# Kernel optimization log

Hardware: AMD Instinct MI355X
Metric: run time of the kernel (lower is better)

The kernel has to match this reference:

```python
import jax, jax.numpy as jnp
import numpy as np

B, TXT_T, MEL_T, N_MEL = 32, 256, 1600, 40
PAD_MAG = 1.0e12


def setup_inputs() -> dict:
    key = jax.random.key(0)
    k1, k2, k3, k4 = jax.random.split(key, 4)
    mu_logvar = jax.random.normal(k1, (B, TXT_T, 2 * N_MEL), jnp.float32)
    z = jax.random.normal(k2, (B, N_MEL, MEL_T), jnp.float32)
    text_lengths = jax.random.randint(k3, (B,), TXT_T // 2, TXT_T + 1).astype(jnp.int32)
    mel_lengths = jax.random.randint(k4, (B,), MEL_T // 2, MEL_T + 1).astype(jnp.int32)
    return {"mu_logvar": mu_logvar, "z": z,
            "text_lengths": text_lengths, "mel_lengths": mel_lengths}


def _mdn_log_prob(mu_logvar, z):
    # mu_logvar: [B, L, 2C], z: [B, C, T] -> log_prob_matrix [B, L, T]
    C = z.shape[1]
    mu, logvar = jnp.split(mu_logvar, 2, axis=-1)          # [B, L, C] each
    invvar = jnp.exp(-logvar)                               # [B, L, C]
    # mean_c((z - mu)^2 * invvar) expanded via matmuls (no [B,L,T,C] tensor)
    t1 = jnp.einsum('bct,blc->blt', z * z, invvar)
    t2 = jnp.einsum('bct,blc->blt', z, mu * invvar)
    t3 = jnp.sum(mu * mu * invvar, axis=-1)[:, :, None]
    mse = t1 - 2.0 * t2 + t3                                # [B, L, T]
    return -0.5 * (mse / C + jnp.mean(logvar, axis=-1)[:, :, None])


def _forward_dp(lp):
    # forward algorithm: log_alpha over (txt position, mel time) via scan over T
    Bb, L, T = lp.shape
    alpha0 = jnp.full((Bb, L + 1), -PAD_MAG, lp.dtype).at[:, 1].set(lp[:, 0, 0])

    def step(alpha, lp_t):
        stay = alpha[:, 1:] + 1e-7
        go = alpha[:, :-1] + 1e-7
        new = jnp.logaddexp(stay, go) + lp_t                # [B, L]
        alpha_new = jnp.concatenate(
            [jnp.full((Bb, 1), -PAD_MAG, lp.dtype), new], axis=1)
        return alpha_new, new

    _, ys = jax.lax.scan(step, alpha0, jnp.moveaxis(lp[:, :, 1:], 2, 0))
    log_alpha = jnp.concatenate([alpha0[:, 1:][None], ys], axis=0)  # [T, B, L]
    return log_alpha


def _viterbi(lp, text_lengths, mel_lengths):
    Bb, L, T = lp.shape
    beta0 = jnp.full((Bb, L), -PAD_MAG, lp.dtype).at[:, 0].set(lp[:, 0, 0])

    def fstep(beta, lp_t):
        shifted = jnp.concatenate(
            [jnp.full((Bb, 1), -PAD_MAG, lp.dtype), beta[:, :-1]], axis=1)
        new = jnp.maximum(beta, shifted) + lp_t
        return new, new

    _, ys = jax.lax.scan(fstep, beta0, jnp.moveaxis(lp[:, :, 1:], 2, 0))
    log_beta = jnp.transpose(jnp.concatenate([beta0[None], ys], axis=0), (1, 2, 0))  # [B, L, T]

    b_idx = jnp.arange(Bb)
    r0 = (text_lengths - 1).astype(jnp.float32)
    c0 = (mel_lengths - 1).astype(jnp.float32)

    def bstep(carry, _):
        rows, cols = carry
        ri = rows.astype(jnp.int32)
        ci = cols.astype(jnp.int32)
        # torch negative indexing wraps -> emulate with mod
        val_go = log_beta[b_idx, (ri - 1) % L, (ci - 1) % T]
        val_stay = log_beta[b_idx, ri % L, (ci - 1) % T]
        is_go = (val_go > val_stay).astype(rows.dtype)
        new_rows = jax.nn.relu(rows - is_go + 1.0) - 1.0
        new_cols = jax.nn.relu(cols) - 1.0
        return (new_rows, new_cols), new_rows

    _, path_ys = jax.lax.scan(bstep, (r0, c0), None, length=T - 1)
    full = jnp.concatenate([r0[None], path_ys], axis=0)     # [T, B], backward order
    path = full[::-1].T                                     # [B, T], chronological
    align = jax.nn.one_hot(path.astype(jnp.int32), L, dtype=lp.dtype)  # [B, T, L]

    def shift(a, ml):
        # F.pad(..., (-pad, pad)) on time axis: shift valid region to the front
        rolled = jnp.roll(a, -(T - ml), axis=0)
        mask = (jnp.arange(T) < ml)[:, None].astype(a.dtype)
        return rolled * mask

    return jax.vmap(shift)(align, mel_lengths)              # [B, T, L]


def reference(mu_logvar, z, text_lengths, mel_lengths):
    lp = _mdn_log_prob(mu_logvar, z)                        # [B, L, T]
    log_alpha = _forward_dp(lp)                             # [T, B, L]
    b_idx = jnp.arange(lp.shape[0])
    alpha_last = log_alpha[mel_lengths - 1, b_idx, text_lengths - 1]
    mdn_loss = -(alpha_last / mel_lengths.astype(alpha_last.dtype))  # [B]
    alignment = _viterbi(lp, text_lengths, mel_lengths)     # [B, T, L]
    return mdn_loss, alignment, lp
```

## Files before the change

kernel.cpp:

```cpp
#include <hip/hip_runtime.h>
#include <cstdint>
#include <math.h>

#define BB   32
#define LLEN 256
#define TLEN 1600
#define NC   40
#define NEGPADF (-1.0e12f)
#define NEGPADD (-1.0e12)
#define NBB   16
#define NBA   32
#define SUBB  8
#define NPROD 4
#define NBUF  3

#define LOG2E_F 1.4426950408889634f
#define LN2_F   0.6931471805599453f
#define C7F     1.4426950408889634e-7f

#define OFF_ALIGN 32
#define OFF_LP    (32 + (size_t)BB * TLEN * LLEN)

#define WSB_A    0
#define WSB_KC   (WSB_A + (size_t)BB * LLEN * 80 * 8)
#define WSB_LPT  (WSB_KC + (size_t)BB * LLEN * 8)

__device__ __forceinline__ int imin(int a, int b) { return a < b ? a : b; }

#define WAIT_LGKM0 0xC07F

__device__ __forceinline__ void bar_prod() {
  asm volatile("" ::: "memory");
  __builtin_amdgcn_s_waitcnt(WAIT_LGKM0);
  __builtin_amdgcn_s_barrier();
  asm volatile("" ::: "memory");
}
__device__ __forceinline__ void bar_cons() {
  asm volatile("" ::: "memory");
  __builtin_amdgcn_s_barrier();
  asm volatile("" ::: "memory");
}

__device__ __forceinline__ int rot1_i32(int x) {
  return __builtin_amdgcn_mov_dpp(x, 0x13C , 0xF, 0xF, true);
}
__device__ __forceinline__ float rot1_f32(float x) {
  return __int_as_float(rot1_i32(__float_as_int(x)));
}
__device__ __forceinline__ double rot1_f64(double x) {
  long long v = __double_as_longlong(x);
  int lo = rot1_i32((int)(v & 0xffffffffLL));
  int hi = rot1_i32((int)(v >> 32));
  return __longlong_as_double(((long long)hi << 32) | (unsigned long long)(unsigned int)lo);
}

__global__ __launch_bounds__(256) void prep_kernel(
    const float* __restrict__ mu_logvar, double* __restrict__ A, double* __restrict__ Kc) {
  int row = blockIdx.x * 4 + (threadIdx.x >> 6);
  int lane = threadIdx.x & 63;
  const float* src = mu_logvar + (size_t)row * (2 * NC);
  double mu = 0.0, lv = 0.0, iv = 0.0, part = 0.0;
  if (lane < NC) {
    mu = (double)src[lane];
    lv = (double)src[NC + lane];
    iv = exp(-lv);
    part = mu * mu * iv + lv;
  }
  for (int m = 1; m < 64; m <<= 1) part += __shfl_xor(part, m, 64);
  const double s = -0.5 / (double)NC;
  if (lane < NC) {
    A[(size_t)row * 80 + lane]      = s * iv;
    A[(size_t)row * 80 + NC + lane] = (1.0 / (double)NC) * mu * iv;
  }
  if (lane == 0) Kc[row] = s * part;
}

__global__ __launch_bounds__(128) void lp_kernel(
    const float* __restrict__ z, const double* __restrict__ A,
    const double* __restrict__ Kc, float* __restrict__ out,
    float* __restrict__ lpTh) {
  int b  = blockIdx.z;
  int l0 = blockIdx.y * 32;
  int t0 = blockIdx.x * 128;
  int tid = threadIdx.x;
  int t = t0 + tid;
  int tv = imin(t, TLEN - 1);
  bool act = (t < TLEN);

  float* lp_out = out + OFF_LP;
  float* loS    = out + OFF_ALIGN;

  float zr[NC];
  const float* zb = z + (size_t)b * NC * TLEN;
  #pragma unroll
  for (int c = 0; c < NC; ++c) zr[c] = zb[(size_t)c * TLEN + tv];

  __shared__ __align__(16) double tile[128][17];
  const double* Ab = A + ((size_t)b * LLEN + l0) * 80;
  const double* Kb = Kc + (size_t)b * LLEN + l0;

  for (int g = 0; g < 2; ++g) {
    for (int j16 = 0; j16 < 16; ++j16) {
      int j = g * 16 + j16;
      const double* Ar = Ab + (size_t)j * 80;
      double a0 = Kb[j], a1 = 0.0, a2 = 0.0, a3 = 0.0;
      #pragma unroll
      for (int c = 0; c < NC; c += 2) {
        double z0 = (double)zr[c], z1 = (double)zr[c + 1];
        a0 = fma(Ar[c],          z0 * z0, a0);
        a1 = fma(Ar[NC + c],     z0,      a1);
        a2 = fma(Ar[c + 1],      z1 * z1, a2);
        a3 = fma(Ar[NC + c + 1], z1,      a3);
      }
      double accd = (a0 + a2) + (a1 + a3);
      if (act) lp_out[((size_t)b * LLEN + l0 + j) * TLEN + t] = (float)accd;
      tile[tid][j16] = accd;
    }
    __syncthreads();
    #pragma unroll
    for (int p = 0; p < 4; ++p) {
      int idx = p * 128 + tid;
      int r = idx >> 2, c4 = idx & 3;
      int tr = t0 + r;
      if (tr < TLEN) {
        float h[4], lo[4];
        #pragma unroll
        for (int i = 0; i < 4; ++i) {
          double d = tile[r][c4 * 4 + i];
          float hh = (float)d;
          h[i] = hh;
          lo[i] = (float)(d - (double)hh);
        }
        size_t base = ((size_t)b * TLEN + tr) * LLEN + l0 + g * 16 + c4 * 4;
        *(float4*)(lpTh + base) = make_float4(h[0], h[1], h[2], h[3]);
        *(float4*)(loS + base)  = make_float4(lo[0], lo[1], lo[2], lo[3]);
      }
    }
    __syncthreads();
  }
}

__global__ __launch_bounds__(320, 1) void dp_kernel(
    const float* __restrict__ lpTh, const float* outR,
    const int* __restrict__ tlen, const int* __restrict__ mlen,
    float* __restrict__ out) {
  int bid = blockIdx.x;
  bool is_beta = (bid >= BB);
  int b = is_beta ? bid - BB : bid;
  int tid = threadIdx.x;
  int lane = tid & 63;
  int wv = tid >> 6;
  int tl = tlen[b];
  int ml = mlen[b];
  const float* lpb = lpTh + (size_t)b * TLEN * LLEN;
  const float* lob = outR + OFF_ALIGN + (size_t)b * TLEN * LLEN;
  float* al = out + OFF_ALIGN + (size_t)b * TLEN * LLEN;
  int nintB = (ml - 2 + NBB) / NBB;
  int nintA = (ml - 2 + NBA) / NBA;

  __shared__ __align__(16) double bufd[NBUF][NBB][4][64];
  __shared__ uint32_t Dbits[LLEN][TLEN / 32];
  __shared__ int pathL[TLEN];
  float* bufaF = (float*)&bufd[0][0][0][0];

  if (wv >= 1) {
    int q = wv - 1;
    const float* ph = lpb + 4 * lane;
    const float* pl = lob + 4 * lane;
    float4 vh[SUBB], vl[SUBB];
    float4 z4 = make_float4(0.f, 0.f, 0.f, 0.f);
    if (!is_beta) {
      int nsb = 4 * nintA;
      auto issueA = [&](int sb) {
        #pragma unroll
        for (int j = 0; j < SUBB; ++j) {
          int c = imin(1 + SUBB * sb + j, TLEN - 1);
          vh[j] = *(const float4*)(ph + (size_t)c * LLEN);
        }
      };
      auto storeA = [&](int sb) {
        int s  = (sb >> 2) % NBUF;
        int jb = (sb & 3) * SUBB;
        #pragma unroll
        for (int j = 0; j < SUBB; ++j) {
          int off = ((s * NBA + jb + j) * 4) * 64 + lane;
          bufaF[off]       = fmaf(vh[j].x, LOG2E_F, C7F);
          bufaF[off + 64]  = fmaf(vh[j].y, LOG2E_F, C7F);
          bufaF[off + 128] = fmaf(vh[j].z, LOG2E_F, C7F);
          bufaF[off + 192] = fmaf(vh[j].w, LOG2E_F, C7F);
        }
      };
      if (q < nsb)     { issueA(q);     storeA(q); }
      if (q + 4 < nsb) { issueA(q + 4); storeA(q + 4); }
      if (q + 8 < nsb) issueA(q + 8);
      bar_prod();
      for (int w = 0; w < nintA; ++w) {
        bar_prod();
        int S = 4 * (w + 2) + q;
        if (S < nsb) {
          storeA(S);
          if (S + 4 < nsb) issueA(S + 4);
        }
      }
    } else {
      int nsb = 2 * nintB;
      auto issueB = [&](int sb) {
        #pragma unroll
        for (int j = 0; j < SUBB; ++j) {
          int c = imin(1 + SUBB * sb + j, TLEN - 1);
          vh[j] = *(const float4*)(ph + (size_t)c * LLEN);
          vl[j] = *(const float4*)(pl + (size_t)c * LLEN);
        }
      };
      auto storeB = [&](int sb) {
        int s  = (sb >> 1) % NBUF;
        int jb = (sb & 1) * SUBB;
        #pragma unroll
        for (int j = 0; j < SUBB; ++j) {
          bufd[s][jb + j][0][lane] = (double)vh[j].x + (double)vl[j].x;
          bufd[s][jb + j][1][lane] = (double)vh[j].y + (double)vl[j].y;
          bufd[s][jb + j][2][lane] = (double)vh[j].z + (double)vl[j].z;
          bufd[s][jb + j][3][lane] = (double)vh[j].w + (double)vl[j].w;
        }
      };
      if (q < nsb) {
        issueB(q); storeB(q);
        if (q + NPROD < nsb) issueB(q + NPROD);
      }
      bar_prod();
      for (int w = 0; w < nintB; ++w) {
        bar_prod();
        int sb0 = 2 * w + 4;
        int mine = ((sb0 & 3) == q) ? sb0 : ((((sb0 + 1) & 3) == q) ? (sb0 + 1) : -1);
        if (mine >= 0 && mine < nsb) {
          storeB(mine);
          if (mine + NPROD < nsb) issueB(mine + NPROD);
        }
        if (w >= 1) {
          int zc = NBB * (w - 1) + 4 * q;
          float* az = al + (size_t)zc * LLEN + 4 * lane;
          #pragma unroll
          for (int k = 0; k < 4; ++k) *(float4*)(az + (size_t)k * LLEN) = z4;
        }
      }
      for (int c = NBB * (nintB - 1) + q; c < TLEN; c += NPROD)
        *(float4*)(al + (size_t)c * LLEN + 4 * lane) = z4;
    }
  } else if (!is_beta) {
    float lp00 = lpb[0] * LOG2E_F;
    float o0 = (lane == 0) ? lp00 : NEGPADF;
    float o1 = NEGPADF, o2 = NEGPADF, o3 = NEGPADF;
    float f0 = o0, f1 = o1, f2 = o2, f3 = o3;
    float qv = rot1_f32(o3);
    bar_cons();
    float P[4][4];
    #pragma unroll
    for (int i = 0; i < 4; ++i) {
      const float* src = bufaF + i * 256;
      P[i][0] = src[lane]; P[i][1] = src[64 + lane];
      P[i][2] = src[128 + lane]; P[i][3] = src[192 + lane];
    }
    int t = 1;
    for (int w = 0; w < nintA; ++w) {
      bar_cons();
      int s = w % NBUF, sn = (w + 1) % NBUF;
      const float* baseS = bufaF + s * (NBA * 256);
      const float* baseN = bufaF + sn * (NBA * 256);
      #pragma unroll
      for (int j = 0; j < NBA; ++j, ++t) {
        int rj = j & 3;
        float l0 = P[rj][0], l1 = P[rj][1], l2 = P[rj][2], l3 = P[rj][3];
        const float* src = (j < NBA - 4) ? (baseS + (j + 4) * 256)
                                         : (baseN + (j + 4 - NBA) * 256);
        P[rj][0] = src[lane];       P[rj][1] = src[64 + lane];
        P[rj][2] = src[128 + lane]; P[rj][3] = src[192 + lane];
        float p = (lane == 0) ? NEGPADF : qv;
        float m0 = fmaxf(o0, p),  d0 = o0 - p;
        float m1 = fmaxf(o1, o0), d1 = o1 - o0;
        float m2 = fmaxf(o2, o1), d2 = o2 - o1;
        float m3 = fmaxf(o3, o2), d3 = o3 - o2;
        float n0 = m0 + __builtin_amdgcn_logf(1.0f + __builtin_amdgcn_exp2f(-fabsf(d0))) + l0;
        float n1 = m1 + __builtin_amdgcn_logf(1.0f + __builtin_amdgcn_exp2f(-fabsf(d1))) + l1;
        float n2 = m2 + __builtin_amdgcn_logf(1.0f + __builtin_amdgcn_exp2f(-fabsf(d2))) + l2;
        float n3 = m3 + __builtin_amdgcn_logf(1.0f + __builtin_amdgcn_exp2f(-fabsf(d3))) + l3;
        o0 = n0; o1 = n1; o2 = n2; o3 = n3;
        qv = rot1_f32(o3);
        if (t == ml - 1) { f0 = o0; f1 = o1; f2 = o2; f3 = o3; }
      }
    }
    int fr = tl - 1;
    if (lane == (fr >> 2)) {
      int sx = fr & 3;
      float val = (sx == 0) ? f0 : (sx == 1) ? f1 : (sx == 2) ? f2 : f3;
      out[b] = -val * LN2_F / (float)ml;
    }
  } else {
    double lp00 = (double)lpb[0] + (double)lob[0];
    double o0 = (lane == 0) ? lp00 : NEGPADD;
    double o1 = NEGPADD, o2 = NEGPADD, o3 = NEGPADD;
    uint32_t a0 = 0, a1 = (lane == 0) ? 1u : 0u, a2 = 0, a3 = 0;
    double qv = rot1_f64(o3);
    bar_cons();
    double P[4][4];
    #pragma unroll
    for (int i = 0; i < 4; ++i) {
      P[i][0] = bufd[0][i][0][lane]; P[i][1] = bufd[0][i][1][lane];
      P[i][2] = bufd[0][i][2][lane]; P[i][3] = bufd[0][i][3][lane];
    }
    int t = 1;
    for (int w = 0; w < nintB; ++w) {
      bar_cons();
      int s = w % NBUF, sn = (w + 1) % NBUF;
      const double (*bs)[4][64] = bufd[s];
      const double (*bn)[4][64] = bufd[sn];
      #pragma unroll
      for (int j = 0; j < NBB; ++j, ++t) {
        int rj = j & 3;
        double l0 = P[rj][0], l1 = P[rj][1], l2 = P[rj][2], l3 = P[rj][3];
        {
          const double (*src)[64] = (j < NBB - 4) ? bs[j + 4] : bn[j + 4 - NBB];
          P[rj][0] = src[0][lane]; P[rj][1] = src[1][lane];
          P[rj][2] = src[2][lane]; P[rj][3] = src[3][lane];
        }
        double p = (lane == 0) ? NEGPADD : qv;
        double n0 = fmax(o0, p)  + l0;
        double n1 = fmax(o1, o0) + l1;
        double n2 = fmax(o2, o1) + l2;
        double n3 = fmax(o3, o2) + l3;
        qv = rot1_f64(n3);
        uint32_t bit = 1u << (t & 31);
        if (qv > n0) a0 |= bit;
        if (n0 > n1) a1 |= bit;
        if (n1 > n2) a2 |= bit;
        if (n2 > n3) a3 |= bit;
        o0 = n0; o1 = n1; o2 = n2; o3 = n3;
        if ((t & 31) == 31) {
          int wd = t >> 5;
          Dbits[4 * lane + 0][wd] = a0; a0 = 0;
          Dbits[4 * lane + 1][wd] = a1; a1 = 0;
          Dbits[4 * lane + 2][wd] = a2; a2 = 0;
          Dbits[4 * lane + 3][wd] = a3; a3 = 0;
        }
      }
    }
    int tend = nintB * NBB;
    int wd = tend >> 5;
    if ((tend & 31) != 31 && wd < TLEN / 32) {
      Dbits[4 * lane + 0][wd] = a0;
      Dbits[4 * lane + 1][wd] = a1;
      Dbits[4 * lane + 2][wd] = a2;
      Dbits[4 * lane + 3][wd] = a3;
    }
    __builtin_amdgcn_s_waitcnt(WAIT_LGKM0);

    if (lane == 0) {
      int r = tl - 1;
      pathL[ml - 1] = r;
      int curR = 1 << 30, curW = -1;
      uint32_t W = 0;
      for (int qq = ml - 2; qq >= 0; --qq) {
        int w2 = qq >> 5;
        if (r >= 0 && (r != curR || w2 != curW)) { W = Dbits[r][w2]; curR = r; curW = w2; }
        int g = (r >= 0) ? (int)((W >> (qq & 31)) & 1u) : 0;
        r -= g;
        pathL[qq] = r;
      }
    }
  }

  if (is_beta) {
    __syncthreads();
    for (int t = tid; t < ml; t += 320) {
      int p = pathL[t];
      if (p >= 0) al[(size_t)t * LLEN + p] = 1.0f;
    }
  }
}

extern "C" void kernel_launch(void* const* d_in, const int* in_sizes, int n_in,
                              void* d_out, int out_size, void* d_ws, size_t ws_size,
                              hipStream_t stream) {
  const float* mu_logvar = (const float*)d_in[0];
  const float* z         = (const float*)d_in[1];
  const int*   tlv       = (const int*)d_in[2];
  const int*   mlv       = (const int*)d_in[3];
  float* out = (float*)d_out;
  char*  wsb = (char*)d_ws;

  double* Ad   = (double*)(wsb + WSB_A);
  double* Kcd  = (double*)(wsb + WSB_KC);
  float*  lpTh = (float*)(wsb + WSB_LPT);

  prep_kernel<<<dim3(BB * LLEN / 4), 256, 0, stream>>>(mu_logvar, Ad, Kcd);
  lp_kernel<<<dim3(13, 8, BB), 128, 0, stream>>>(z, Ad, Kcd, out, lpTh);
  dp_kernel<<<dim3(2 * BB), 320, 0, stream>>>(lpTh, out, tlv, mlv, out);
}
```

Measured before the change: 496.5 us.

## Replace producer/consumer barriers with LDS flag polling in DP kernel

Swaps the workgroup-wide s_barrier handshakes between the four producer waves and the consumer wave for per-producer progress counters and a consumer progress counter in LDS. Each side spin-waits with s_sleep on those counters. The forward (alpha) path also drops its 32-step window and uses the same 16-step window and sub-block indexing as the Viterbi path. The goal is to let producers run ahead and stop the serial DP wave stalling at every window barrier. The cost is polling overhead and a dependence on volatile LDS ordering being correct.

```diff
diff --git a/kernel.cpp b/kernel.cpp
--- a/kernel.cpp
+++ b/kernel.cpp
@@ -9,7 +9,6 @@
 #define NEGPADF (-1.0e12f)
 #define NEGPADD (-1.0e12)
 #define NBB   16
-#define NBA   32
 #define SUBB  8
 #define NPROD 4
 #define NBUF  3
@@ -28,18 +27,6 @@
 __device__ __forceinline__ int imin(int a, int b) { return a < b ? a : b; }
 
 #define WAIT_LGKM0 0xC07F
-
-__device__ __forceinline__ void bar_prod() {
-  asm volatile("" ::: "memory");
-  __builtin_amdgcn_s_waitcnt(WAIT_LGKM0);
-  __builtin_amdgcn_s_barrier();
-  asm volatile("" ::: "memory");
-}
-__device__ __forceinline__ void bar_cons() {
-  asm volatile("" ::: "memory");
-  __builtin_amdgcn_s_barrier();
-  asm volatile("" ::: "memory");
-}
 
 __device__ __forceinline__ int rot1_i32(int x) {
   return __builtin_amdgcn_mov_dpp(x, 0x13C , 0xF, 0xF, true);
@@ -155,13 +142,19 @@
   const float* lpb = lpTh + (size_t)b * TLEN * LLEN;
   const float* lob = outR + OFF_ALIGN + (size_t)b * TLEN * LLEN;
   float* al = out + OFF_ALIGN + (size_t)b * TLEN * LLEN;
-  int nintB = (ml - 2 + NBB) / NBB;
-  int nintA = (ml - 2 + NBA) / NBA;
+  int nint = (ml - 2 + NBB) / NBB;
+  int nsb  = 2 * nint;
 
   __shared__ __align__(16) double bufd[NBUF][NBB][4][64];
   __shared__ uint32_t Dbits[LLEN][TLEN / 32];
   __shared__ int pathL[TLEN];
+  __shared__ int prodSb_s[NPROD];
+  __shared__ int consW_s;
   float* bufaF = (float*)&bufd[0][0][0][0];
+
+  if (tid < NPROD) prodSb_s[tid] = 0;
+  if (tid == NPROD) consW_s = 0;
+  __syncthreads();
 
   if (wv >= 1) {
     int q = wv - 1;
@@ -169,8 +162,8 @@
     const float* pl = lob + 4 * lane;
     float4 vh[SUBB], vl[SUBB];
     float4 z4 = make_float4(0.f, 0.f, 0.f, 0.f);
+    int myCnt = 0;
     if (!is_beta) {
-      int nsb = 4 * nintA;
       auto issueA = [&](int sb) {
         #pragma unroll
         for (int j = 0; j < SUBB; ++j) {
@@ -179,31 +172,33 @@
         }
       };
       auto storeA = [&](int sb) {
-        int s  = (sb >> 2) % NBUF;
-        int jb = (sb & 3) * SUBB;
+        int s  = (sb >> 1) % NBUF;
+        int jb = (sb & 1) * SUBB;
         #pragma unroll
         for (int j = 0; j < SUBB; ++j) {
-          int off = ((s * NBA + jb + j) * 4) * 64 + lane;
+          int off = ((s * NBB + jb + j) * 4) * 64 + lane;
           bufaF[off]       = fmaf(vh[j].x, LOG2E_F, C7F);
           bufaF[off + 64]  = fmaf(vh[j].y, LOG2E_F, C7F);
           bufaF[off + 128] = fmaf(vh[j].z, LOG2E_F, C7F);
           bufaF[off + 192] = fmaf(vh[j].w, LOG2E_F, C7F);
         }
       };
-      if (q < nsb)     { issueA(q);     storeA(q); }
-      if (q + 4 < nsb) { issueA(q + 4); storeA(q + 4); }
-      if (q + 8 < nsb) issueA(q + 8);
-      bar_prod();
-      for (int w = 0; w < nintA; ++w) {
-        bar_prod();
-        int S = 4 * (w + 2) + q;
-        if (S < nsb) {
-          storeA(S);
-          if (S + 4 < nsb) issueA(S + 4);
-        }
+      if (q < nsb) issueA(q);
+      for (int sb = q; sb < nsb; sb += 4) {
+        int u = sb >> 1;
+        if (u >= 3) {
+          while (*(volatile int*)&consW_s < u - 2) __builtin_amdgcn_s_sleep(2);
+        }
+        asm volatile("" ::: "memory");
+        storeA(sb);
+        asm volatile("" ::: "memory");
+        __builtin_amdgcn_s_waitcnt(WAIT_LGKM0);
+        ++myCnt;
+        if (lane == 0) *(volatile int*)&prodSb_s[q] = myCnt;
+        asm volatile("" ::: "memory");
+        if (sb + 4 < nsb) issueA(sb + 4);
       }
     } else {
-      int nsb = 2 * nintB;
       auto issueB = [&](int sb) {
         #pragma unroll
         for (int j = 0; j < SUBB; ++j) {
@@ -223,147 +218,168 @@
           bufd[s][jb + j][3][lane] = (double)vh[j].w + (double)vl[j].w;
         }
       };
-      if (q < nsb) {
-        issueB(q); storeB(q);
-        if (q + NPROD < nsb) issueB(q + NPROD);
-      }
-      bar_prod();
-      for (int w = 0; w < nintB; ++w) {
-        bar_prod();
-        int sb0 = 2 * w + 4;
-        int mine = ((sb0 & 3) == q) ? sb0 : ((((sb0 + 1) & 3) == q) ? (sb0 + 1) : -1);
-        if (mine >= 0 && mine < nsb) {
-          storeB(mine);
-          if (mine + NPROD < nsb) issueB(mine + NPROD);
-        }
-        if (w >= 1) {
-          int zc = NBB * (w - 1) + 4 * q;
+      if (q < nsb) issueB(q);
+      for (int sb = q; sb < nsb; sb += 4) {
+        int u = sb >> 1;
+        if (u >= 3) {
+          while (*(volatile int*)&consW_s < u - 2) __builtin_amdgcn_s_sleep(2);
+        }
+        asm volatile("" ::: "memory");
+        storeB(sb);
+        asm volatile("" ::: "memory");
+        __builtin_amdgcn_s_waitcnt(WAIT_LGKM0);
+        ++myCnt;
+        if (lane == 0) *(volatile int*)&prodSb_s[q] = myCnt;
+        asm volatile("" ::: "memory");
+        if (sb + 4 < nsb) issueB(sb + 4);
+        if (u >= 2) {
+          int zc = NBB * (u - 2) + 8 * (q & 1);
           float* az = al + (size_t)zc * LLEN + 4 * lane;
           #pragma unroll
-          for (int k = 0; k < 4; ++k) *(float4*)(az + (size_t)k * LLEN) = z4;
-        }
-      }
-      for (int c = NBB * (nintB - 1) + q; c < TLEN; c += NPROD)
+          for (int k = 0; k < 8; ++k) *(float4*)(az + (size_t)k * LLEN) = z4;
+        }
+      }
+      for (int c = NBB * (nint - 2) + q; c < TLEN; c += NPROD)
         *(float4*)(al + (size_t)c * LLEN + 4 * lane) = z4;
     }
-  } else if (!is_beta) {
-    float lp00 = lpb[0] * LOG2E_F;
-    float o0 = (lane == 0) ? lp00 : NEGPADF;
-    float o1 = NEGPADF, o2 = NEGPADF, o3 = NEGPADF;
-    float f0 = o0, f1 = o1, f2 = o2, f3 = o3;
-    float qv = rot1_f32(o3);
-    bar_cons();
-    float P[4][4];
-    #pragma unroll
-    for (int i = 0; i < 4; ++i) {
-      const float* src = bufaF + i * 256;
-      P[i][0] = src[lane]; P[i][1] = src[64 + lane];
-      P[i][2] = src[128 + lane]; P[i][3] = src[192 + lane];
-    }
-    int t = 1;
-    for (int w = 0; w < nintA; ++w) {
-      bar_cons();
-      int s = w % NBUF, sn = (w + 1) % NBUF;
-      const float* baseS = bufaF + s * (NBA * 256);
-      const float* baseN = bufaF + sn * (NBA * 256);
+  } else {
+    auto pollC = [&](int X) {
+      for (;;) {
+        int m0 = 0 + 4 * *(volatile int*)&prodSb_s[0];
+        int m1 = 1 + 4 * *(volatile int*)&prodSb_s[1];
+        int m2 = 2 + 4 * *(volatile int*)&prodSb_s[2];
+        int m3 = 3 + 4 * *(volatile int*)&prodSb_s[3];
+        if (imin(imin(m0, m1), imin(m2, m3)) >= X) break;
+        __builtin_amdgcn_s_sleep(1);
+      }
+      asm volatile("" ::: "memory");
+    };
+    auto publish = [&](int w1) {
+      asm volatile("" ::: "memory");
+      if (lane == 0) *(volatile int*)&consW_s = w1;
+      asm volatile("" ::: "memory");
+    };
+    if (!is_beta) {
+      float lp00 = lpb[0] * LOG2E_F;
+      float o0 = (lane == 0) ? lp00 : NEGPADF;
+      float o1 = NEGPADF, o2 = NEGPADF, o3 = NEGPADF;
+      float f0 = o0, f1 = o1, f2 = o2, f3 = o3;
+      float qv = rot1_f32(o3);
+      pollC(imin(4, nsb));
+      float P[4][4];
       #pragma unroll
-      for (int j = 0; j < NBA; ++j, ++t) {
-        int rj = j & 3;
-        float l0 = P[rj][0], l1 = P[rj][1], l2 = P[rj][2], l3 = P[rj][3];
-        const float* src = (j < NBA - 4) ? (baseS + (j + 4) * 256)
-                                         : (baseN + (j + 4 - NBA) * 256);
-        P[rj][0] = src[lane];       P[rj][1] = src[64 + lane];
-        P[rj][2] = src[128 + lane]; P[rj][3] = src[192 + lane];
-        float p = (lane == 0) ? NEGPADF : qv;
-        float m0 = fmaxf(o0, p),  d0 = o0 - p;
-        float m1 = fmaxf(o1, o0), d1 = o1 - o0;
-        float m2 = fmaxf(o2, o1), d2 = o2 - o1;
-        float m3 = fmaxf(o3, o2), d3 = o3 - o2;
-        float n0 = m0 + __builtin_amdgcn_logf(1.0f + __builtin_amdgcn_exp2f(-fabsf(d0))) + l0;
-        float n1 = m1 + __builtin_amdgcn_logf(1.0f + __builtin_amdgcn_exp2f(-fabsf(d1))) + l1;
-        float n2 = m2 + __builtin_amdgcn_logf(1.0f + __builtin_amdgcn_exp2f(-fabsf(d2))) + l2;
-        float n3 = m3 + __builtin_amdgcn_logf(1.0f + __builtin_amdgcn_exp2f(-fabsf(d3))) + l3;
-        o0 = n0; o1 = n1; o2 = n2; o3 = n3;
-        qv = rot1_f32(o3);
-        if (t == ml - 1) { f0 = o0; f1 = o1; f2 = o2; f3 = o3; }
-      }
-    }
-    int fr = tl - 1;
-    if (lane == (fr >> 2)) {
-      int sx = fr & 3;
-      float val = (sx == 0) ? f0 : (sx == 1) ? f1 : (sx == 2) ? f2 : f3;
-      out[b] = -val * LN2_F / (float)ml;
-    }
-  } else {
-    double lp00 = (double)lpb[0] + (double)lob[0];
-    double o0 = (lane == 0) ? lp00 : NEGPADD;
-    double o1 = NEGPADD, o2 = NEGPADD, o3 = NEGPADD;
-    uint32_t a0 = 0, a1 = (lane == 0) ? 1u : 0u, a2 = 0, a3 = 0;
-    double qv = rot1_f64(o3);
-    bar_cons();
-    double P[4][4];
-    #pragma unroll
-    for (int i = 0; i < 4; ++i) {
-      P[i][0] = bufd[0][i][0][lane]; P[i][1] = bufd[0][i][1][lane];
-      P[i][2] = bufd[0][i][2][lane]; P[i][3] = bufd[0][i][3][lane];
-    }
-    int t = 1;
-    for (int w = 0; w < nintB; ++w) {
-      bar_cons();
-      int s = w % NBUF, sn = (w + 1) % NBUF;
-      const double (*bs)[4][64] = bufd[s];
-      const double (*bn)[4][64] = bufd[sn];
+      for (int i = 0; i < 4; ++i) {
+        const float* src = bufaF + i * 256;
+        P[i][0] = src[lane]; P[i][1] = src[64 + lane];
+        P[i][2] = src[128 + lane]; P[i][3] = src[192 + lane];
+      }
+      int t = 1;
+      for (int w = 0; w < nint; ++w) {
+        if (w) pollC(imin(2 * w + 4, nsb));
+        int s = w % NBUF, sn = (w + 1) % NBUF;
+        const float* baseS = bufaF + s * (NBB * 256);
+        const float* baseN = bufaF + sn * (NBB * 256);
+        #pragma unroll
+        for (int j = 0; j < NBB; ++j, ++t) {
+          int rj = j & 3;
+          float l0 = P[rj][0], l1 = P[rj][1], l2 = P[rj][2], l3 = P[rj][3];
+          const float* src = (j < NBB - 4) ? (baseS + (j + 4) * 256)
+                                           : (baseN + (j + 4 - NBB) * 256);
+          P[rj][0] = src[lane];       P[rj][1] = src[64 + lane];
+          P[rj][2] = src[128 + lane]; P[rj][3] = src[192 + lane];
+          float p = (lane == 0) ? NEGPADF : qv;
+          float m0 = fmaxf(o0, p),  d0 = o0 - p;
+          float m1 = fmaxf(o1, o0), d1 = o1 - o0;
+          float m2 = fmaxf(o2, o1), d2 = o2 - o1;
+          float m3 = fmaxf(o3, o2), d3 = o3 - o2;
+          float n0 = m0 + __builtin_amdgcn_logf(1.0f + __builtin_amdgcn_exp2f(-fabsf(d0))) + l0;
+          float n1 = m1 + __builtin_amdgcn_logf(1.0f + __builtin_amdgcn_exp2f(-fabsf(d1))) + l1;
+          float n2 = m2 + __builtin_amdgcn_logf(1.0f + __builtin_amdgcn_exp2f(-fabsf(d2))) + l2;
+          float n3 = m3 + __builtin_amdgcn_logf(1.0f + __builtin_amdgcn_exp2f(-fabsf(d3))) + l3;
+          o0 = n0; o1 = n1; o2 = n2; o3 = n3;
+          qv = rot1_f32(o3);
+          if (t == ml - 1) { f0 = o0; f1 = o1; f2 = o2; f3 = o3; }
+        }
+        publish(w + 1);
+      }
+      int fr = tl - 1;
+      if (lane == (fr >> 2)) {
+        int sx = fr & 3;
+        float val = (sx == 0) ? f0 : (sx == 1) ? f1 : (sx == 2) ? f2 : f3;
+        out[b] = -val * LN2_F / (float)ml;
+      }
+    } else {
+      double lp00 = (double)lpb[0] + (double)lob[0];
+      double o0 = (lane == 0) ? lp00 : NEGPADD;
+      double o1 = NEGPADD, o2 = NEGPADD, o3 = NEGPADD;
+      uint32_t a0 = 0, a1 = (lane == 0) ? 1u : 0u, a2 = 0, a3 = 0;
+      double qv = rot1_f64(o3);
+      pollC(imin(4, nsb));
+      double P[4][4];
       #pragma unroll
-      for (int j = 0; j < NBB; ++j, ++t) {
-        int rj = j & 3;
-        double l0 = P[rj][0], l1 = P[rj][1], l2 = P[rj][2], l3 = P[rj][3];
-        {
-          const double (*src)[64] = (j < NBB - 4) ? bs[j + 4] : bn[j + 4 - NBB];
-          P[rj][0] = src[0][lane]; P[rj][1] = src[1][lane];
-          P[rj][2] = src[2][lane]; P[rj][3] = src[3][lane];
-        }
-        double p = (lane == 0) ? NEGPADD : qv;
-        double n0 = fmax(o0, p)  + l0;
-        double n1 = fmax(o1, o0) + l1;
-        double n2 = fmax(o2, o1) + l2;
-        double n3 = fmax(o3, o2) + l3;
-        qv = rot1_f64(n3);
-        uint32_t bit = 1u << (t & 31);
-        if (qv > n0) a0 |= bit;
-        if (n0 > n1) a1 |= bit;
-        if (n1 > n2) a2 |= bit;
-        if (n2 > n3) a3 |= bit;
-        o0 = n0; o1 = n1; o2 = n2; o3 = n3;
-        if ((t & 31) == 31) {
-          int wd = t >> 5;
-          Dbits[4 * lane + 0][wd] = a0; a0 = 0;
-          Dbits[4 * lane + 1][wd] = a1; a1 = 0;
-          Dbits[4 * lane + 2][wd] = a2; a2 = 0;
-          Dbits[4 * lane + 3][wd] = a3; a3 = 0;
-        }
-      }
-    }
-    int tend = nintB * NBB;
-    int wd = tend >> 5;
-    if ((tend & 31) != 31 && wd < TLEN / 32) {
-      Dbits[4 * lane + 0][wd] = a0;
-      Dbits[4 * lane + 1][wd] = a1;
-      Dbits[4 * lane + 2][wd] = a2;
-      Dbits[4 * lane + 3][wd] = a3;
-    }
-    __builtin_amdgcn_s_waitcnt(WAIT_LGKM0);
-
-    if (lane == 0) {
-      int r = tl - 1;
-      pathL[ml - 1] = r;
-      int curR = 1 << 30, curW = -1;
-      uint32_t W = 0;
-      for (int qq = ml - 2; qq >= 0; --qq) {
-        int w2 = qq >> 5;
-        if (r >= 0 && (r != curR || w2 != curW)) { W = Dbits[r][w2]; curR = r; curW = w2; }
-        int g = (r >= 0) ? (int)((W >> (qq & 31)) & 1u) : 0;
-        r -= g;
-        pathL[qq] = r;
+      for (int i = 0; i < 4; ++i) {
+        P[i][0] = bufd[0][i][0][lane]; P[i][1] = bufd[0][i][1][lane];
+        P[i][2] = bufd[0][i][2][lane]; P[i][3] = bufd[0][i][3][lane];
+      }
+      int t = 1;
+      for (int w = 0; w < nint; ++w) {
+        if (w) pollC(imin(2 * w + 4, nsb));
+        int s = w % NBUF, sn = (w + 1) % NBUF;
+        const double (*bs)[4][64] = bufd[s];
+        const double (*bn)[4][64] = bufd[sn];
+        #pragma unroll
+        for (int j = 0; j < NBB; ++j, ++t) {
+          int rj = j & 3;
+          double l0 = P[rj][0], l1 = P[rj][1], l2 = P[rj][2], l3 = P[rj][3];
+          {
+            const double (*src)[64] = (j < NBB - 4) ? bs[j + 4] : bn[j + 4 - NBB];
+            P[rj][0] = src[0][lane]; P[rj][1] = src[1][lane];
+            P[rj][2] = src[2][lane]; P[rj][3] = src[3][lane];
+          }
+          double p = (lane == 0) ? NEGPADD : qv;
+          double n0 = fmax(o0, p)  + l0;
+          double n1 = fmax(o1, o0) + l1;
+          double n2 = fmax(o2, o1) + l2;
+          double n3 = fmax(o3, o2) + l3;
+          qv = rot1_f64(n3);
+          uint32_t bit = 1u << (t & 31);
+          if (qv > n0) a0 |= bit;
+          if (n0 > n1) a1 |= bit;
+          if (n1 > n2) a2 |= bit;
+          if (n2 > n3) a3 |= bit;
+          o0 = n0; o1 = n1; o2 = n2; o3 = n3;
+          if ((t & 31) == 31) {
+            int wd = t >> 5;
+            Dbits[4 * lane + 0][wd] = a0; a0 = 0;
+            Dbits[4 * lane + 1][wd] = a1; a1 = 0;
+            Dbits[4 * lane + 2][wd] = a2; a2 = 0;
+            Dbits[4 * lane + 3][wd] = a3; a3 = 0;
+          }
+        }
+        publish(w + 1);
+      }
+      int tend = nint * NBB;
+      int wd = tend >> 5;
+      if ((tend & 31) != 31 && wd < TLEN / 32) {
+        Dbits[4 * lane + 0][wd] = a0;
+        Dbits[4 * lane + 1][wd] = a1;
+        Dbits[4 * lane + 2][wd] = a2;
+        Dbits[4 * lane + 3][wd] = a3;
+      }
+      __builtin_amdgcn_s_waitcnt(WAIT_LGKM0);
+
+      if (lane == 0) {
+        int r = tl - 1;
+        pathL[ml - 1] = r;
+        int curR = 1 << 30, curW = -1;
+        uint32_t W = 0;
+        for (int qq = ml - 2; qq >= 0; --qq) {
+          int w2 = qq >> 5;
+          if (r >= 0 && (r != curR || w2 != curW)) { W = Dbits[r][w2]; curR = r; curW = w2; }
+          int g = (r >= 0) ? (int)((W >> (qq & 31)) & 1u) : 0;
+          r -= g;
+          pathL[qq] = r;
+        }
       }
     }
   }
```

Result: slower. 550.7 us (+10.9%).
